# Kernel tuning notes

Hardware: AMD Instinct MI355X
Metric: run time of the kernel (lower is better)

The kernel has to match this reference:

```python
import jax, jax.numpy as jnp
import numpy as np

B, N, D = 8, 64, 512          # batch, latent tokens, token dim
C, H, W, P = 256, 128, 128, 36  # img feat channels/HW, sampling points
PG = 128                       # parameter-generator inner dim (0.25*D)
HEADS = 8                      # D // 64
TOT = C * C + P * P            # adaptive mixing param count per token


def _ln(x, g, b):
    m = x.mean(-1, keepdims=True)
    v = x.var(-1, keepdims=True)
    return (x - m) / jnp.sqrt(v + 1e-5) * g + b


def _gelu(x):
    return jax.nn.gelu(x, approximate=False)


def _grid_sample(img, grid):
    # img: (B,C,H,W); grid: (B,N,P,2) in [-1,1]; bilinear, border pad, align_corners=False
    Bi, Ci, Hi, Wi = img.shape
    x = ((grid[..., 0] + 1.0) * Wi - 1.0) * 0.5
    y = ((grid[..., 1] + 1.0) * Hi - 1.0) * 0.5
    x0 = jnp.floor(x)
    y0 = jnp.floor(y)
    wx = x - x0
    wy = y - y0
    x0i = jnp.clip(x0.astype(jnp.int32), 0, Wi - 1)
    x1i = jnp.clip(x0.astype(jnp.int32) + 1, 0, Wi - 1)
    y0i = jnp.clip(y0.astype(jnp.int32), 0, Hi - 1)
    y1i = jnp.clip(y0.astype(jnp.int32) + 1, 0, Hi - 1)
    imgt = img.transpose(0, 2, 3, 1)  # (B,H,W,C)
    bidx = jnp.arange(Bi)[:, None, None]
    v00 = imgt[bidx, y0i, x0i]  # (B,N,P,C)
    v01 = imgt[bidx, y0i, x1i]
    v10 = imgt[bidx, y1i, x0i]
    v11 = imgt[bidx, y1i, x1i]
    wx = wx[..., None]
    wy = wy[..., None]
    return (v00 * (1 - wx) * (1 - wy) + v01 * wx * (1 - wy)
            + v10 * (1 - wx) * wy + v11 * wx * wy)


def setup_inputs() -> dict:
    key = jax.random.key(0)
    ks = jax.random.split(key, 16)
    rn = lambda k, s, sc: jax.random.normal(k, s, jnp.float32) * sc
    tl = jax.random.uniform(ks[0], (B, N, 2), jnp.float32) * 0.5
    wh = 0.2 + jax.random.uniform(ks[1], (B, N, 2), jnp.float32) * 0.4
    return dict(
        token_embed=rn(ks[2], (B, N, D), 1.0),
        token_roi=jnp.concatenate([tl, tl + wh], axis=-1),
        img_feat=rn(ks[3], (B, C, H, W), 1.0),
        ln_off_g=jnp.ones(D), ln_off_b=jnp.zeros(D),
        w_off=rn(ks[4], (D, P * 2), D ** -0.5),
        roi_offset_bias=rn(ks[5], (P * 2,), 1.0),
        ln_pg_g=jnp.ones(D), ln_pg_b=jnp.zeros(D),
        w_pg1=rn(ks[6], (D, PG), D ** -0.5), b_pg1=jnp.zeros(PG),
        w_pg2=rn(ks[7], (PG, TOT), 0.02 * PG ** -0.5),
        b_pg2=rn(ks[8], (TOT,), 0.02),
        m_beta=jnp.zeros(C), s_beta=jnp.zeros(P),
        w_out=rn(ks[9], (P * C, D), (P * C) ** -0.5), b_out=jnp.zeros(D),
        ln1_g=jnp.ones(D), ln1_b=jnp.zeros(D),
        w_qkv=rn(ks[10], (D, 3 * D), D ** -0.5), b_qkv=jnp.zeros(3 * D),
        w_proj=rn(ks[11], (D, D), D ** -0.5), b_proj=jnp.zeros(D),
        ln2_g=jnp.ones(D), ln2_b=jnp.zeros(D),
        w_fc1=rn(ks[12], (D, 4 * D), D ** -0.5), b_fc1=jnp.zeros(4 * D),
        w_fc2=rn(ks[13], (4 * D, D), (4 * D) ** -0.5), b_fc2=jnp.zeros(D),
    )


def reference(token_embed, token_roi, img_feat,
              ln_off_g, ln_off_b, w_off, roi_offset_bias,
              ln_pg_g, ln_pg_b, w_pg1, b_pg1, w_pg2, b_pg2,
              m_beta, s_beta, w_out, b_out,
              ln1_g, ln1_b, w_qkv, b_qkv, w_proj, b_proj,
              ln2_g, ln2_b, w_fc1, b_fc1, w_fc2, b_fc2):
    Bq, Nq, Dm = token_embed.shape
    # --- OP.SAMPLING_M: offsets -> absolute points (n_heads=1) ---
    off = _ln(token_embed, ln_off_g, ln_off_b) @ w_off + roi_offset_bias  # (B,N,2P)
    off = off.reshape(Bq, Nq, 1, P, 2)
    mu = off.mean(-2, keepdims=True)
    sd = jnp.std(off, axis=-2, keepdims=True, ddof=1) + 1e-5  # unbiased, as torch.std
    off = (off - mu) / (3.0 * sd)
    xy = (token_roi[..., 2:] + token_roi[..., :2]) * 0.5
    wh = token_roi[..., 2:] - token_roi[..., :2]
    pts = xy[:, :, None, None, :] + off * wh[:, :, None, None, :]  # (B,N,1,P,2)
    grid = pts.reshape(Bq, Nq, P, 2) * 2.0 - 1.0
    sampled = _grid_sample(img_feat, grid)  # (B,N,P,C)
    # --- adaptive mixing (AdaMixer): per-token generated channel/spatial weights ---
    q = _ln(token_embed, ln_pg_g, ln_pg_b)
    params = (q @ w_pg1 + b_pg1) @ w_pg2 + b_pg2  # (B,N,TOT)
    cm = params[..., :C * C].reshape(Bq, Nq, C, C)
    sm = params[..., C * C:].reshape(Bq, Nq, P, P)
    h = _gelu(jnp.einsum('bnpc,bncd->bnpd', sampled, cm) + m_beta)
    h = _gelu(jnp.einsum('bnqp,bnpd->bnqd', sm, h) + s_beta[:, None])
    token_embed = token_embed + (h.reshape(Bq, Nq, P * C) @ w_out + b_out)
    # --- OP.ATTN ---
    x = _ln(token_embed, ln1_g, ln1_b)
    hd = Dm // HEADS
    qkv = (x @ w_qkv + b_qkv).reshape(Bq, Nq, 3, HEADS, hd)
    qh, kh, vh = qkv[:, :, 0], qkv[:, :, 1], qkv[:, :, 2]
    att = jax.nn.softmax(jnp.einsum('bqhd,bkhd->bhqk', qh, kh) * hd ** -0.5, axis=-1)
    o = jnp.einsum('bhqk,bkhd->bqhd', att, vh).reshape(Bq, Nq, Dm)
    token_embed = token_embed + (o @ w_proj + b_proj)
    # --- OP.MLP ---
    x = _ln(token_embed, ln2_g, ln2_b)
    token_embed = token_embed + (_gelu(x @ w_fc1 + b_fc1) @ w_fc2 + b_fc2)
    return token_embed
```

## Files before the change

kernel.cpp:

```cpp
#include <hip/hip_runtime.h>
#include <hip/hip_bf16.h>

typedef __hip_bfloat16 bf16;
typedef __attribute__((ext_vector_type(8))) short short8;
typedef __attribute__((ext_vector_type(4))) float f32x4;

#define NTOK 512
#define TOTC 66832
#define CM_SZ 65536

__device__ __forceinline__ float b2f(bf16 x) { return __bfloat162float(x); }
__device__ __forceinline__ bf16 f2b(float x) { return __float2bfloat16(x); }
__device__ __forceinline__ float gelu_f(float x) {
  return 0.5f * x * (1.0f + erff(x * 0.7071067811865476f));
}
__device__ __forceinline__ f32x4 mfma16(short8 a, short8 b, f32x4 c) {
  return __builtin_amdgcn_mfma_f32_16x16x32_bf16(a, b, c, 0, 0, 0);
}

__global__ __launch_bounds__(256) void k_transpose(const float* __restrict__ img,
                                                   bf16* __restrict__ imgT) {
  int b = blockIdx.y;
  int hw0 = blockIdx.x * 32;
  __shared__ float tile[256][33];
  int t = threadIdx.x;
  int hw = t & 31, c0 = t >> 5;
#pragma unroll 8
  for (int i = 0; i < 32; ++i) {
    int c = c0 + 8 * i;
    tile[c][hw] = img[((size_t)(b * 256 + c) << 14) + hw0 + hw];
  }
  __syncthreads();
#pragma unroll 8
  for (int i = 0; i < 32; ++i) {
    imgT[(((size_t)b << 14) + hw0 + i) * 256 + t] = f2b(tile[t][i]);
  }
}

__global__ __launch_bounds__(256) void k_prep(
    const float* __restrict__ te, const float* __restrict__ roi,
    const float* __restrict__ g_off, const float* __restrict__ b_off,
    const float* __restrict__ w_off, const float* __restrict__ off_bias,
    const float* __restrict__ g_pg, const float* __restrict__ b_pg,
    const float* __restrict__ w_pg1, const float* __restrict__ b_pg1,
    bf16* __restrict__ t_out, int* __restrict__ meta_i, float* __restrict__ meta_w) {
  int tok = blockIdx.x;
  int t = threadIdx.x, lane = t & 63, w = t >> 6;
  __shared__ float xo[512], xq[512], offb[72], red[4], wsum[4];
  size_t base = (size_t)tok * 512;
  float a0 = te[base + t];
  float a1 = te[base + t + 256];
  float s = a0 + a1;
#pragma unroll
  for (int o = 32; o; o >>= 1) s += __shfl_xor(s, o);
  if (lane == 0) wsum[w] = s;
  __syncthreads();
  float mean = (wsum[0] + wsum[1] + wsum[2] + wsum[3]) * (1.0f / 512.0f);
  float d0 = a0 - mean, d1 = a1 - mean;
  float ss = d0 * d0 + d1 * d1;
#pragma unroll
  for (int o = 32; o; o >>= 1) ss += __shfl_xor(ss, o);
  __syncthreads();
  if (lane == 0) wsum[w] = ss;
  __syncthreads();
  float var = (wsum[0] + wsum[1] + wsum[2] + wsum[3]) * (1.0f / 512.0f);
  float rstd = rsqrtf(var + 1e-5f);
  xo[t] = d0 * rstd * g_off[t] + b_off[t];
  xo[t + 256] = d1 * rstd * g_off[t + 256] + b_off[t + 256];
  xq[t] = d0 * rstd * g_pg[t] + b_pg[t];
  xq[t + 256] = d1 * rstd * g_pg[t + 256] + b_pg[t + 256];
  __syncthreads();
  if (t < 128) {
    float acc = b_pg1[t];
    for (int d = 0; d < 512; ++d) acc = fmaf(xq[d], w_pg1[d * 128 + t], acc);
    t_out[(size_t)tok * 128 + t] = f2b(acc);
  } else if (t < 200) {
    int j = t - 128;
    float acc = off_bias[j];
    for (int d = 0; d < 512; ++d) acc = fmaf(xo[d], w_off[d * 72 + j], acc);
    offb[j] = acc;
  }
  __syncthreads();
  if (t < 2) {
    float mu = 0.f;
    for (int p = 0; p < 36; ++p) mu += offb[p * 2 + t];
    mu *= (1.0f / 36.0f);
    float s2 = 0.f;
    for (int p = 0; p < 36; ++p) { float dd = offb[p * 2 + t] - mu; s2 += dd * dd; }
    float sd = sqrtf(s2 * (1.0f / 35.0f)) + 1e-5f;
    red[t] = mu;
    red[2 + t] = 1.0f / (3.0f * sd);
  }
  __syncthreads();
  if (t < 36) {
    int p = t;
    float r0 = roi[tok * 4 + 0], r1 = roi[tok * 4 + 1];
    float r2 = roi[tok * 4 + 2], r3 = roi[tok * 4 + 3];
    float cx = (r0 + r2) * 0.5f, cy = (r1 + r3) * 0.5f;
    float bw = r2 - r0, bh = r3 - r1;
    float ox = (offb[p * 2 + 0] - red[0]) * red[2];
    float oy = (offb[p * 2 + 1] - red[1]) * red[3];
    float fx = (cx + ox * bw) * 128.0f - 0.5f;
    float fy = (cy + oy * bh) * 128.0f - 0.5f;
    float x0f = floorf(fx), y0f = floorf(fy);
    float wx = fx - x0f, wy = fy - y0f;
    int x0 = min(max((int)x0f, 0), 127);
    int x1 = min(max((int)x0f + 1, 0), 127);
    int y0 = min(max((int)y0f, 0), 127);
    int y1 = min(max((int)y0f + 1, 0), 127);
    int ibase = (tok >> 6) * 16384;
    int mi = (tok * 36 + p) * 4;
    meta_i[mi + 0] = (ibase + y0 * 128 + x0) * 256;
    meta_i[mi + 1] = (ibase + y0 * 128 + x1) * 256;
    meta_i[mi + 2] = (ibase + y1 * 128 + x0) * 256;
    meta_i[mi + 3] = (ibase + y1 * 128 + x1) * 256;
    meta_w[mi + 0] = (1.f - wx) * (1.f - wy);
    meta_w[mi + 1] = wx * (1.f - wy);
    meta_w[mi + 2] = (1.f - wx) * wy;
    meta_w[mi + 3] = wx * wy;
  }
}

__global__ __launch_bounds__(256) void k_sample(const bf16* __restrict__ imgT,
                                                const int* __restrict__ meta_i,
                                                const float* __restrict__ meta_w,
                                                bf16* __restrict__ S) {
  int tok = blockIdx.x, t = threadIdx.x;
  for (int p = 0; p < 36; ++p) {
    int mi = (tok * 36 + p) * 4;
    int o00 = meta_i[mi + 0], o01 = meta_i[mi + 1], o10 = meta_i[mi + 2], o11 = meta_i[mi + 3];
    float w00 = meta_w[mi + 0], w01 = meta_w[mi + 1], w10 = meta_w[mi + 2], w11 = meta_w[mi + 3];
    float v = w00 * b2f(imgT[o00 + t]) + w01 * b2f(imgT[o01 + t]) +
              w10 * b2f(imgT[o10 + t]) + w11 * b2f(imgT[o11 + t]);
    S[((size_t)tok * 36 + p) * 256 + t] = f2b(v);
  }
}

__global__ __launch_bounds__(256) void k_wt(const float* __restrict__ w0, bf16* __restrict__ o0,
                                            const float* __restrict__ w1, bf16* __restrict__ o1,
                                            const float* __restrict__ w2, bf16* __restrict__ o2,
                                            const float* __restrict__ w3, bf16* __restrict__ o3,
                                            const float* __restrict__ w4, bf16* __restrict__ o4) {
  int b = blockIdx.x;
  const float* W;
  bf16* O;
  int K, N, loc;
  if (b < 4608) { W = w0; O = o0; K = 9216; N = 512; loc = b; }
  else if (b < 5376) { W = w1; O = o1; K = 512; N = 1536; loc = b - 4608; }
  else if (b < 5632) { W = w2; O = o2; K = 512; N = 512; loc = b - 5376; }
  else if (b < 6656) { W = w3; O = o3; K = 512; N = 2048; loc = b - 5632; }
  else { W = w4; O = o4; K = 2048; N = 512; loc = b - 6656; }
  int ntn = N >> 5;
  int nb = loc % ntn, kb = loc / ntn;
  int n0 = nb * 32, k0 = kb * 32;
  __shared__ float tl[32][33];
  int t = threadIdx.x, r = t >> 5, c = t & 31;
#pragma unroll
  for (int i = 0; i < 4; ++i)
    tl[r + 8 * i][c] = W[(size_t)(k0 + r + 8 * i) * N + n0 + c];
  __syncthreads();
#pragma unroll
  for (int i = 0; i < 4; ++i)
    O[(size_t)(n0 + r + 8 * i) * K + k0 + c] = f2b(tl[c][r + 8 * i]);
}

__global__ __launch_bounds__(256) void k_pg2_mfma(const bf16* __restrict__ tb16,
                                                  const float* __restrict__ w2,
                                                  const float* __restrict__ b2,
                                                  bf16* __restrict__ pchunk) {
  int n0 = blockIdx.x * 64;
  int row0 = blockIdx.y * 256;
  int t = threadIdx.x, lane = t & 63, w = t >> 6;
  int quad = lane >> 4, l16 = lane & 15;
  __shared__ bf16 BsT[64][136];
  {
    int nl = (t & 15) * 4, kk = t >> 4;
#pragma unroll
    for (int pass = 0; pass < 8; ++pass) {
      int k = kk + pass * 16;
      int n = n0 + nl;
      int nc = (n + 3 < TOTC) ? n : (TOTC - 4);
      const float4 v = *(const float4*)(w2 + (size_t)k * TOTC + nc);
      BsT[nl + 0][k] = f2b(v.x);
      BsT[nl + 1][k] = f2b(v.y);
      BsT[nl + 2][k] = f2b(v.z);
      BsT[nl + 3][k] = f2b(v.w);
    }
  }
  __syncthreads();
  f32x4 acc[4][4];
#pragma unroll
  for (int i = 0; i < 4; ++i)
#pragma unroll
    for (int j = 0; j < 4; ++j) acc[i][j] = (f32x4){0.f, 0.f, 0.f, 0.f};
  const bf16* Abase = tb16 + ((size_t)(row0 + w * 64 + l16)) * 128 + quad * 8;
#pragma unroll
  for (int ks = 0; ks < 4; ++ks) {
    short8 af[4], bff[4];
#pragma unroll
    for (int mt = 0; mt < 4; ++mt)
      af[mt] = *(const short8*)(Abase + mt * 16 * 128 + ks * 32);
#pragma unroll
    for (int nt = 0; nt < 4; ++nt)
      bff[nt] = *(const short8*)(&BsT[nt * 16 + l16][ks * 32 + quad * 8]);
#pragma unroll
    for (int mt = 0; mt < 4; ++mt)
#pragma unroll
      for (int nt = 0; nt < 4; ++nt)
        acc[mt][nt] = mfma16(af[mt], bff[nt], acc[mt][nt]);
  }
#pragma unroll
  for (int nt = 0; nt < 4; ++nt) {
    int col = n0 + nt * 16 + l16;
    if (col >= TOTC) continue;
    float bias = b2[col];
#pragma unroll
    for (int mt = 0; mt < 4; ++mt) {
      int r0 = row0 + w * 64 + mt * 16 + quad * 4;
#pragma unroll
      for (int r = 0; r < 4; ++r)
        pchunk[(size_t)(r0 + r) * TOTC + col] = f2b(acc[mt][nt][r] + bias);
    }
  }
}

__global__ __launch_bounds__(256) void k_cmT(const bf16* __restrict__ pchunk,
                                             bf16* __restrict__ pcmT) {
  int tok = blockIdx.y;
  int c0 = (blockIdx.x & 3) * 64, d0 = (blockIdx.x >> 2) * 64;
  __shared__ bf16 tl[64][72];
  int t = threadIdx.x;
  {
    int c = t >> 2, dl = (t & 3) * 16;
    const bf16* src = pchunk + (size_t)tok * TOTC + (size_t)(c0 + c) * 256 + d0 + dl;
    *(short8*)&tl[c][dl] = *(const short8*)src;
    *(short8*)&tl[c][dl + 8] = *(const short8*)(src + 8);
  }
  __syncthreads();
  {
    int dr = t & 63, cc = (t >> 6) * 16;
    bf16 tmp[16];
#pragma unroll
    for (int i = 0; i < 16; ++i) tmp[i] = tl[cc + i][dr];
    bf16* dst = pcmT + (size_t)tok * 65536 + (size_t)(d0 + dr) * 256 + c0 + cc;
    *(short8*)dst = *(const short8*)tmp;
    *(short8*)(dst + 8) = *(const short8*)(tmp + 8);
  }
}

__global__ __launch_bounds__(256) void k_mix3(const bf16* __restrict__ pchunk,
                                              const bf16* __restrict__ pcmT,
                                              const bf16* __restrict__ S,
                                              const float* __restrict__ m_beta,
                                              const float* __restrict__ s_beta,
                                              bf16* __restrict__ h2) {
  int tok = blockIdx.x, dh = blockIdx.y * 128;
  int t = threadIdx.x, lane = t & 63, w = t >> 6;
  int quad = lane >> 4, l16 = lane & 15;
  __shared__ bf16 h1T[128][72];
  __shared__ bf16 smS[48][72];
  for (int i = t; i < 1728; i += 256) ((unsigned*)smS)[i] = 0u;
  __syncthreads();
  const bf16* sm = pchunk + (size_t)tok * TOTC + CM_SZ;
  for (int i = t; i < 1296; i += 256) {
    int q = i / 36, p = i - q * 36;
    smS[q][p] = sm[i];
  }
  f32x4 acc[3][2];
#pragma unroll
  for (int i = 0; i < 3; ++i)
#pragma unroll
    for (int j = 0; j < 2; ++j) acc[i][j] = (f32x4){0.f, 0.f, 0.f, 0.f};
  const bf16* Sg = S + (size_t)tok * 9216;
  const bf16* Cg = pcmT + (size_t)tok * 65536;
  int dw = w * 32;
#pragma unroll
  for (int kc = 0; kc < 256; kc += 32) {
    short8 a[3], b[2];
#pragma unroll
    for (int mt = 0; mt < 3; ++mt)
      a[mt] = *(const short8*)(Sg + (size_t)(mt * 16 + l16) * 256 + kc + quad * 8);
#pragma unroll
    for (int nt = 0; nt < 2; ++nt)
      b[nt] = *(const short8*)(Cg + (size_t)(dh + dw + nt * 16 + l16) * 256 + kc + quad * 8);
#pragma unroll
    for (int mt = 0; mt < 3; ++mt)
#pragma unroll
      for (int nt = 0; nt < 2; ++nt)
        acc[mt][nt] = mfma16(a[mt], b[nt], acc[mt][nt]);
  }
#pragma unroll
  for (int nt = 0; nt < 2; ++nt) {
    int dl = dw + nt * 16 + l16;
    float mb = m_beta[dh + dl];
#pragma unroll
    for (int mt = 0; mt < 3; ++mt)
#pragma unroll
      for (int r = 0; r < 4; ++r) {
        int p = mt * 16 + quad * 4 + r;
        if (p < 36) h1T[dl][p] = f2b(gelu_f(acc[mt][nt][r] + mb));
      }
  }
  for (int i = t; i < 128 * 28; i += 256) {
    int d = i / 28, p = 36 + i % 28;
    h1T[d][p] = (bf16)0.f;
  }
  __syncthreads();
  f32x4 acc2[3][2];
#pragma unroll
  for (int i = 0; i < 3; ++i)
#pragma unroll
    for (int j = 0; j < 2; ++j) acc2[i][j] = (f32x4){0.f, 0.f, 0.f, 0.f};
#pragma unroll
  for (int ks = 0; ks < 2; ++ks) {
    short8 a2[3], b2v[2];
#pragma unroll
    for (int mt = 0; mt < 3; ++mt)
      a2[mt] = *(const short8*)&smS[mt * 16 + l16][ks * 32 + quad * 8];
#pragma unroll
    for (int nt = 0; nt < 2; ++nt)
      b2v[nt] = *(const short8*)&h1T[dw + nt * 16 + l16][ks * 32 + quad * 8];
#pragma unroll
    for (int mt = 0; mt < 3; ++mt)
#pragma unroll
      for (int nt = 0; nt < 2; ++nt)
        acc2[mt][nt] = mfma16(a2[mt], b2v[nt], acc2[mt][nt]);
  }
  bf16* h2p = h2 + (size_t)tok * 9216 + dh;
#pragma unroll
  for (int mt = 0; mt < 3; ++mt)
#pragma unroll
    for (int r = 0; r < 4; ++r) {
      int q = mt * 16 + quad * 4 + r;
      if (q >= 36) continue;
      float sb = s_beta[q];
#pragma unroll
      for (int nt = 0; nt < 2; ++nt)
        h2p[q * 256 + dw + nt * 16 + l16] = f2b(gelu_f(acc2[mt][nt][r] + sb));
    }
}

__global__ __launch_bounds__(256) void k_gemm_bt(const bf16* __restrict__ A,
                                                 const bf16* __restrict__ BT,
                                                 float* __restrict__ part,
                                                 int M, int N, int K) {
  int nb = blockIdx.x, mb = blockIdx.y, ks = blockIdx.z;
  int kchunk = K / gridDim.z;
  int k0 = ks * kchunk;
  __shared__ bf16 As[64][72], Bs[64][72];
  int t = threadIdx.x, lane = t & 63, w = t >> 6;
  int quad = lane >> 4, l16 = lane & 15;
  int wm = (w >> 1) * 32, wn = (w & 1) * 32;
  int r = t >> 2, kk = (t & 3) * 16;
  f32x4 acc[2][2];
#pragma unroll
  for (int i = 0; i < 2; ++i)
#pragma unroll
    for (int j = 0; j < 2; ++j) acc[i][j] = (f32x4){0.f, 0.f, 0.f, 0.f};
  for (int kt = 0; kt < kchunk; kt += 64) {
    __syncthreads();
    const bf16* ga = A + (size_t)(mb * 64 + r) * K + k0 + kt + kk;
    *(short8*)&As[r][kk] = *(const short8*)ga;
    *(short8*)&As[r][kk + 8] = *(const short8*)(ga + 8);
    const bf16* gb = BT + (size_t)(nb * 64 + r) * K + k0 + kt + kk;
    *(short8*)&Bs[r][kk] = *(const short8*)gb;
    *(short8*)&Bs[r][kk + 8] = *(const short8*)(gb + 8);
    __syncthreads();
#pragma unroll
    for (int kss = 0; kss < 2; ++kss) {
      short8 af[2], bff[2];
#pragma unroll
      for (int mt = 0; mt < 2; ++mt)
        af[mt] = *(const short8*)&As[wm + mt * 16 + l16][kss * 32 + quad * 8];
#pragma unroll
      for (int nt = 0; nt < 2; ++nt)
        bff[nt] = *(const short8*)&Bs[wn + nt * 16 + l16][kss * 32 + quad * 8];
#pragma unroll
      for (int mt = 0; mt < 2; ++mt)
#pragma unroll
        for (int nt = 0; nt < 2; ++nt)
          acc[mt][nt] = mfma16(af[mt], bff[nt], acc[mt][nt]);
    }
  }
#pragma unroll
  for (int mt = 0; mt < 2; ++mt)
#pragma unroll
    for (int rr = 0; rr < 4; ++rr) {
      int m = mb * 64 + wm + mt * 16 + quad * 4 + rr;
#pragma unroll
      for (int nt = 0; nt < 2; ++nt) {
        int n = nb * 64 + wn + nt * 16 + l16;
        part[(size_t)ks * M * N + (size_t)m * N + n] = acc[mt][nt][rr];
      }
    }
}

__global__ __launch_bounds__(256) void k_epi(const float* __restrict__ part, int S_,
                                             int MN, int N, const float* __restrict__ bias,
                                             const float* __restrict__ resf, int do_gelu,
                                             float* __restrict__ outf, bf16* __restrict__ outh) {
  int idx = blockIdx.x * 256 + threadIdx.x;
  if (idx >= MN) return;
  int n = idx % N;
  float a = 0.f;
  for (int s = 0; s < S_; ++s) a += part[(size_t)s * MN + idx];
  a += bias[n];
  if (resf) a += resf[idx];
  if (do_gelu) a = gelu_f(a);
  if (outf) outf[idx] = a;
  if (outh) outh[idx] = f2b(a);
}

__global__ __launch_bounds__(256) void k_ln(const float* __restrict__ x,
                                            const float* __restrict__ g,
                                            const float* __restrict__ b,
                                            bf16* __restrict__ out) {
  int tok = blockIdx.x, t = threadIdx.x, lane = t & 63, w = t >> 6;
  __shared__ float wsum[4];
  size_t base = (size_t)tok * 512;
  float a0 = x[base + t], a1 = x[base + t + 256];
  float s = a0 + a1;
#pragma unroll
  for (int o = 32; o; o >>= 1) s += __shfl_xor(s, o);
  if (lane == 0) wsum[w] = s;
  __syncthreads();
  float mean = (wsum[0] + wsum[1] + wsum[2] + wsum[3]) * (1.0f / 512.0f);
  float d0 = a0 - mean, d1 = a1 - mean;
  float ss = d0 * d0 + d1 * d1;
#pragma unroll
  for (int o = 32; o; o >>= 1) ss += __shfl_xor(ss, o);
  __syncthreads();
  if (lane == 0) wsum[w] = ss;
  __syncthreads();
  float var = (wsum[0] + wsum[1] + wsum[2] + wsum[3]) * (1.0f / 512.0f);
  float rstd = rsqrtf(var + 1e-5f);
  out[base + t] = f2b(d0 * rstd * g[t] + b[t]);
  out[base + t + 256] = f2b(d1 * rstd * g[t + 256] + b[t + 256]);
}

__global__ __launch_bounds__(256) void k_attn(const float* __restrict__ qkvf,
                                              bf16* __restrict__ obuf) {
  int b = blockIdx.x >> 3, h = blockIdx.x & 7;
  __shared__ float kT[64][65];
  __shared__ float vT[64][65];
  __shared__ float att[64][65];
  int t = threadIdx.x, lane = t & 63, w = t >> 6;
#pragma unroll
  for (int i = 0; i < 16; ++i) {
    int idx = t + i * 256;
    int j = idx >> 6, d = idx & 63;
    size_t tb = (size_t)(b * 64 + j) * 1536 + h * 64 + d;
    kT[j][d] = qkvf[tb + 512];
    vT[j][d] = qkvf[tb + 1024];
  }
  __syncthreads();
#pragma unroll 4
  for (int m = 0; m < 16; ++m) {
    int i = w * 16 + m;
    const float* qrow = &qkvf[(size_t)(b * 64 + i) * 1536 + h * 64];
    float s = 0.f;
    for (int d = 0; d < 64; ++d) s = fmaf(qrow[d], kT[lane][d], s);
    s *= 0.125f;
    float mx = s;
#pragma unroll
    for (int o = 32; o; o >>= 1) mx = fmaxf(mx, __shfl_xor(mx, o));
    float e = expf(s - mx);
    float sum = e;
#pragma unroll
    for (int o = 32; o; o >>= 1) sum += __shfl_xor(sum, o);
    att[i][lane] = e / sum;
  }
  __syncthreads();
#pragma unroll 4
  for (int m = 0; m < 16; ++m) {
    int i = w * 16 + m;
    float o = 0.f;
    for (int j = 0; j < 64; ++j) o = fmaf(att[i][j], vT[j][lane], o);
    obuf[(size_t)(b * 64 + i) * 512 + h * 64 + lane] = f2b(o);
  }
}

extern "C" void kernel_launch(void* const* d_in, const int* in_sizes, int n_in,
                              void* d_out, int out_size, void* d_ws, size_t ws_size,
                              hipStream_t stream) {
  const float* te = (const float*)d_in[0];
  const float* roi = (const float*)d_in[1];
  const float* img = (const float*)d_in[2];
  const float* ln_off_g = (const float*)d_in[3];
  const float* ln_off_b = (const float*)d_in[4];
  const float* w_off = (const float*)d_in[5];
  const float* off_bias = (const float*)d_in[6];
  const float* ln_pg_g = (const float*)d_in[7];
  const float* ln_pg_b = (const float*)d_in[8];
  const float* w_pg1 = (const float*)d_in[9];
  const float* b_pg1 = (const float*)d_in[10];
  const float* w_pg2 = (const float*)d_in[11];
  const float* b_pg2 = (const float*)d_in[12];
  const float* m_beta = (const float*)d_in[13];
  const float* s_beta = (const float*)d_in[14];
  const float* w_out = (const float*)d_in[15];
  const float* b_out = (const float*)d_in[16];
  const float* ln1_g = (const float*)d_in[17];
  const float* ln1_b = (const float*)d_in[18];
  const float* w_qkv = (const float*)d_in[19];
  const float* b_qkv = (const float*)d_in[20];
  const float* w_proj = (const float*)d_in[21];
  const float* b_proj = (const float*)d_in[22];
  const float* ln2_g = (const float*)d_in[23];
  const float* ln2_b = (const float*)d_in[24];
  const float* w_fc1 = (const float*)d_in[25];
  const float* b_fc1 = (const float*)d_in[26];
  const float* w_fc2 = (const float*)d_in[27];
  const float* b_fc2 = (const float*)d_in[28];

  char* ws = (char*)d_ws;
  bf16* imgT = (bf16*)ws;
  char* ov = ws;
  bf16* h2 = (bf16*)ov; ov += 9437184;
  float* part = (float*)ov; ov += 8388608;
  float* x1 = (float*)ov; ov += 1048576;
  float* xa = (float*)ov; ov += 1048576;
  float* qkvf = (float*)ov; ov += 3145728;
  bf16* ln1buf = (bf16*)ov; ov += 524288;
  bf16* ln2buf = (bf16*)ov; ov += 524288;
  bf16* obuf = (bf16*)ov; ov += 524288;
  bf16* hfc = (bf16*)ov; ov += 2097152;
  char* tail = ws + 67108864;
  bf16* Sbuf = (bf16*)tail; tail += 9437184;
  bf16* tb16 = (bf16*)tail; tail += 131072;
  int* meta_i = (int*)tail; tail += 294912;
  float* meta_w = (float*)tail; tail += 294912;
  bf16* pchunk = (bf16*)tail; tail += (size_t)NTOK * TOTC * 2;
  bf16* pcmT = (bf16*)tail; tail += (size_t)NTOK * 65536 * 2;
  bf16* w_outT = (bf16*)tail; tail += 9437184;
  bf16* w_qkvT = (bf16*)tail; tail += 1572864;
  bf16* w_projT = (bf16*)tail; tail += 524288;
  bf16* w_fc1T = (bf16*)tail; tail += 2097152;
  bf16* w_fc2T = (bf16*)tail; tail += 2097152;
  (void)ws_size;

  k_transpose<<<dim3(512, 8), 256, 0, stream>>>(img, imgT);
  k_prep<<<512, 256, 0, stream>>>(te, roi, ln_off_g, ln_off_b, w_off, off_bias,
                                  ln_pg_g, ln_pg_b, w_pg1, b_pg1, tb16, meta_i, meta_w);
  k_sample<<<512, 256, 0, stream>>>(imgT, meta_i, meta_w, Sbuf);
  k_wt<<<7680, 256, 0, stream>>>(w_out, w_outT, w_qkv, w_qkvT, w_proj, w_projT,
                                 w_fc1, w_fc1T, w_fc2, w_fc2T);
  k_pg2_mfma<<<dim3(1045, 2), 256, 0, stream>>>(tb16, w_pg2, b_pg2, pchunk);
  k_cmT<<<dim3(16, 512), 256, 0, stream>>>(pchunk, pcmT);
  k_mix3<<<dim3(512, 2), 256, 0, stream>>>(pchunk, pcmT, Sbuf, m_beta, s_beta, h2);

  k_gemm_bt<<<dim3(8, 8, 8), 256, 0, stream>>>(h2, w_outT, part, 512, 512, 9216);
  k_epi<<<1024, 256, 0, stream>>>(part, 8, 512 * 512, 512, b_out, te, 0, x1, nullptr);

  k_ln<<<512, 256, 0, stream>>>(x1, ln1_g, ln1_b, ln1buf);
  k_gemm_bt<<<dim3(24, 8, 2), 256, 0, stream>>>(ln1buf, w_qkvT, part, 512, 1536, 512);
  k_epi<<<3072, 256, 0, stream>>>(part, 2, 512 * 1536, 1536, b_qkv, nullptr, 0, qkvf, nullptr);
  k_attn<<<64, 256, 0, stream>>>(qkvf, obuf);
  k_gemm_bt<<<dim3(8, 8, 4), 256, 0, stream>>>(obuf, w_projT, part, 512, 512, 512);
  k_epi<<<1024, 256, 0, stream>>>(part, 4, 512 * 512, 512, b_proj, x1, 0, xa, nullptr);

  k_ln<<<512, 256, 0, stream>>>(xa, ln2_g, ln2_b, ln2buf);
  k_gemm_bt<<<dim3(32, 8, 2), 256, 0, stream>>>(ln2buf, w_fc1T, part, 512, 2048, 512);
  k_epi<<<4096, 256, 0, stream>>>(part, 2, 512 * 2048, 2048, b_fc1, nullptr, 1, nullptr, hfc);
  k_gemm_bt<<<dim3(8, 8, 4), 256, 0, stream>>>(hfc, w_fc2T, part, 512, 512, 2048);
  k_epi<<<1024, 256, 0, stream>>>(part, 4, 512 * 512, 512, b_fc2, xa, 0, (float*)d_out, nullptr);
}
```

Baseline: 573.2 us.

## Fuse channel-mix transpose into mix kernel and fuse split-K epilogue with LayerNorm

The separate k_cmT transpose kernel and its 64 MB intermediate buffer are removed. k_mix3 now reads the untransposed channel-mix weights from pchunk with register prefetch of the next K-chunk, and transposes them through a per-wave LDS tile before feeding MFMA. The split-K reduction, bias and residual epilogues before each LayerNorm are fused into a single k_epi_ln kernel, saving two launches and one round trip of activations. A sample-loop unroll pragma is also added. The LDS transpose uses scalar short stores, which may cause bank conflicts and adds LDS pressure.

```diff
diff --git a/kernel.cpp b/kernel.cpp
--- a/kernel.cpp
+++ b/kernel.cpp
@@ -126,6 +126,7 @@
                                                 const float* __restrict__ meta_w,
                                                 bf16* __restrict__ S) {
   int tok = blockIdx.x, t = threadIdx.x;
+#pragma unroll 6
   for (int p = 0; p < 36; ++p) {
     int mi = (tok * 36 + p) * 4;
     int o00 = meta_i[mi + 0], o01 = meta_i[mi + 1], o10 = meta_i[mi + 2], o11 = meta_i[mi + 3];
@@ -224,32 +225,7 @@
   }
 }
 
-__global__ __launch_bounds__(256) void k_cmT(const bf16* __restrict__ pchunk,
-                                             bf16* __restrict__ pcmT) {
-  int tok = blockIdx.y;
-  int c0 = (blockIdx.x & 3) * 64, d0 = (blockIdx.x >> 2) * 64;
-  __shared__ bf16 tl[64][72];
-  int t = threadIdx.x;
-  {
-    int c = t >> 2, dl = (t & 3) * 16;
-    const bf16* src = pchunk + (size_t)tok * TOTC + (size_t)(c0 + c) * 256 + d0 + dl;
-    *(short8*)&tl[c][dl] = *(const short8*)src;
-    *(short8*)&tl[c][dl + 8] = *(const short8*)(src + 8);
-  }
-  __syncthreads();
-  {
-    int dr = t & 63, cc = (t >> 6) * 16;
-    bf16 tmp[16];
-#pragma unroll
-    for (int i = 0; i < 16; ++i) tmp[i] = tl[cc + i][dr];
-    bf16* dst = pcmT + (size_t)tok * 65536 + (size_t)(d0 + dr) * 256 + c0 + cc;
-    *(short8*)dst = *(const short8*)tmp;
-    *(short8*)(dst + 8) = *(const short8*)(tmp + 8);
-  }
-}
-
 __global__ __launch_bounds__(256) void k_mix3(const bf16* __restrict__ pchunk,
-                                              const bf16* __restrict__ pcmT,
                                               const bf16* __restrict__ S,
                                               const float* __restrict__ m_beta,
                                               const float* __restrict__ s_beta,
@@ -259,6 +235,7 @@
   int quad = lane >> 4, l16 = lane & 15;
   __shared__ bf16 h1T[128][72];
   __shared__ bf16 smS[48][72];
+  __shared__ short cmw[4][32][40];
   for (int i = t; i < 1728; i += 256) ((unsigned*)smS)[i] = 0u;
   __syncthreads();
   const bf16* sm = pchunk + (size_t)tok * TOTC + CM_SZ;
@@ -272,22 +249,42 @@
 #pragma unroll
     for (int j = 0; j < 2; ++j) acc[i][j] = (f32x4){0.f, 0.f, 0.f, 0.f};
   const bf16* Sg = S + (size_t)tok * 9216;
-  const bf16* Cg = pcmT + (size_t)tok * 65536;
+  const bf16* Cg = pchunk + (size_t)tok * TOTC;
   int dw = w * 32;
+  int c_l = lane & 31;
+  int dtop = (lane >> 5) * 16;
+  const bf16* src0 = Cg + (size_t)c_l * 256 + dh + dw + dtop;
+  short8 v0 = *(const short8*)src0;
+  short8 v1 = *(const short8*)(src0 + 8);
 #pragma unroll
   for (int kc = 0; kc < 256; kc += 32) {
-    short8 a[3], b[2];
+#pragma unroll
+    for (int j = 0; j < 8; ++j) cmw[w][dtop + j][c_l] = v0[j];
+#pragma unroll
+    for (int j = 0; j < 8; ++j) cmw[w][dtop + 8 + j][c_l] = v1[j];
+    short8 a[3];
 #pragma unroll
     for (int mt = 0; mt < 3; ++mt)
       a[mt] = *(const short8*)(Sg + (size_t)(mt * 16 + l16) * 256 + kc + quad * 8);
+    short8 v0n, v1n;
+    if (kc < 224) {
+      const bf16* srcn = Cg + (size_t)(kc + 32 + c_l) * 256 + dh + dw + dtop;
+      v0n = *(const short8*)srcn;
+      v1n = *(const short8*)(srcn + 8);
+    }
+    asm volatile("" ::: "memory");
+    short8 bfr[2];
 #pragma unroll
     for (int nt = 0; nt < 2; ++nt)
-      b[nt] = *(const short8*)(Cg + (size_t)(dh + dw + nt * 16 + l16) * 256 + kc + quad * 8);
+      bfr[nt] = *(const short8*)&cmw[w][nt * 16 + l16][quad * 8];
 #pragma unroll
     for (int mt = 0; mt < 3; ++mt)
 #pragma unroll
       for (int nt = 0; nt < 2; ++nt)
-        acc[mt][nt] = mfma16(a[mt], b[nt], acc[mt][nt]);
+        acc[mt][nt] = mfma16(a[mt], bfr[nt], acc[mt][nt]);
+    asm volatile("" ::: "memory");
+    v0 = v0n;
+    v1 = v1n;
   }
 #pragma unroll
   for (int nt = 0; nt < 2; ++nt) {
@@ -411,14 +408,25 @@
   if (outh) outh[idx] = f2b(a);
 }
 
-__global__ __launch_bounds__(256) void k_ln(const float* __restrict__ x,
-                                            const float* __restrict__ g,
-                                            const float* __restrict__ b,
-                                            bf16* __restrict__ out) {
+__global__ __launch_bounds__(256) void k_epi_ln(const float* __restrict__ part, int S_,
+                                                const float* __restrict__ bias,
+                                                const float* __restrict__ res,
+                                                const float* __restrict__ g,
+                                                const float* __restrict__ bvec,
+                                                float* __restrict__ xout,
+                                                bf16* __restrict__ lnout) {
   int tok = blockIdx.x, t = threadIdx.x, lane = t & 63, w = t >> 6;
   __shared__ float wsum[4];
   size_t base = (size_t)tok * 512;
-  float a0 = x[base + t], a1 = x[base + t + 256];
+  float a0 = bias[t] + res[base + t];
+  float a1 = bias[t + 256] + res[base + t + 256];
+  for (int sp = 0; sp < S_; ++sp) {
+    const float* p = part + (size_t)sp * 262144 + base;
+    a0 += p[t];
+    a1 += p[t + 256];
+  }
+  xout[base + t] = a0;
+  xout[base + t + 256] = a1;
   float s = a0 + a1;
 #pragma unroll
   for (int o = 32; o; o >>= 1) s += __shfl_xor(s, o);
@@ -434,8 +442,8 @@
   __syncthreads();
   float var = (wsum[0] + wsum[1] + wsum[2] + wsum[3]) * (1.0f / 512.0f);
   float rstd = rsqrtf(var + 1e-5f);
-  out[base + t] = f2b(d0 * rstd * g[t] + b[t]);
-  out[base + t + 256] = f2b(d1 * rstd * g[t + 256] + b[t + 256]);
+  lnout[base + t] = f2b(d0 * rstd * g[t] + bvec[t]);
+  lnout[base + t + 256] = f2b(d1 * rstd * g[t + 256] + bvec[t + 256]);
 }
 
 __global__ __launch_bounds__(256) void k_attn(const float* __restrict__ qkvf,
@@ -531,7 +539,6 @@
   int* meta_i = (int*)tail; tail += 294912;
   float* meta_w = (float*)tail; tail += 294912;
   bf16* pchunk = (bf16*)tail; tail += (size_t)NTOK * TOTC * 2;
-  bf16* pcmT = (bf16*)tail; tail += (size_t)NTOK * 65536 * 2;
   bf16* w_outT = (bf16*)tail; tail += 9437184;
   bf16* w_qkvT = (bf16*)tail; tail += 1572864;
   bf16* w_projT = (bf16*)tail; tail += 524288;
@@ -546,20 +553,17 @@
   k_wt<<<7680, 256, 0, stream>>>(w_out, w_outT, w_qkv, w_qkvT, w_proj, w_projT,
                                  w_fc1, w_fc1T, w_fc2, w_fc2T);
   k_pg2_mfma<<<dim3(1045, 2), 256, 0, stream>>>(tb16, w_pg2, b_pg2, pchunk);
-  k_cmT<<<dim3(16, 512), 256, 0, stream>>>(pchunk, pcmT);
-  k_mix3<<<dim3(512, 2), 256, 0, stream>>>(pchunk, pcmT, Sbuf, m_beta, s_beta, h2);
+  k_mix3<<<dim3(512, 2), 256, 0, stream>>>(pchunk, Sbuf, m_beta, s_beta, h2);
 
   k_gemm_bt<<<dim3(8, 8, 8), 256, 0, stream>>>(h2, w_outT, part, 512, 512, 9216);
-  k_epi<<<1024, 256, 0, stream>>>(part, 8, 512 * 512, 512, b_out, te, 0, x1, nullptr);
-
-  k_ln<<<512, 256, 0, stream>>>(x1, ln1_g, ln1_b, ln1buf);
+  k_epi_ln<<<512, 256, 0, stream>>>(part, 8, b_out, te, ln1_g, ln1_b, x1, ln1buf);
+
   k_gemm_bt<<<dim3(24, 8, 2), 256, 0, stream>>>(ln1buf, w_qkvT, part, 512, 1536, 512);
   k_epi<<<3072, 256, 0, stream>>>(part, 2, 512 * 1536, 1536, b_qkv, nullptr, 0, qkvf, nullptr);
   k_attn<<<64, 256, 0, stream>>>(qkvf, obuf);
   k_gemm_bt<<<dim3(8, 8, 4), 256, 0, stream>>>(obuf, w_projT, part, 512, 512, 512);
-  k_epi<<<1024, 256, 0, stream>>>(part, 4, 512 * 512, 512, b_proj, x1, 0, xa, nullptr);
-
-  k_ln<<<512, 256, 0, stream>>>(xa, ln2_g, ln2_b, ln2buf);
+  k_epi_ln<<<512, 256, 0, stream>>>(part, 4, b_proj, x1, ln2_g, ln2_b, xa, ln2buf);
+
   k_gemm_bt<<<dim3(32, 8, 2), 256, 0, stream>>>(ln2buf, w_fc1T, part, 512, 2048, 512);
   k_epi<<<4096, 256, 0, stream>>>(part, 2, 512 * 2048, 2048, b_fc1, nullptr, 1, nullptr, hfc);
   k_gemm_bt<<<dim3(8, 8, 4), 256, 0, stream>>>(hfc, w_fc2T, part, 512, 512, 2048);
```

New measurement: 537.0 us. 6.3% less time.
